# Kernel tuning notes

Hardware: AMD Instinct MI355X
Metric: run time of the kernel (lower is better)

Reference implementation:

```python
import jax, jax.numpy as jnp
import numpy as np
import math

N = 100000
E = 800000
H = 256
TDIM = 32
NTYPES = 22
NLAYERS = 2


def layer_norm(x, g, b, eps=1e-5):
    mu = jnp.mean(x, axis=-1, keepdims=True)
    var = jnp.var(x, axis=-1, keepdims=True)
    return (x - mu) * jax.lax.rsqrt(var + eps) * g + b


def setup_inputs() -> dict:
    key = jax.random.key(0)
    ks = jax.random.split(key, 16)
    s = 1.0 / math.sqrt(H)
    inp = {
        "clause_reprs": jax.random.normal(ks[0], (N, H), dtype=jnp.float32),
        "timestamps": jax.random.uniform(ks[1], (N,), dtype=jnp.float32) * 10000.0,
        "deriv_types": jax.random.randint(ks[2], (N,), 0, NTYPES),
        "derivation_edges": jax.random.randint(ks[3], (2, E), 0, N),
        # params
        "emb_table": jax.random.normal(ks[4], (NTYPES, H), dtype=jnp.float32),
        "temp_W": jax.random.normal(ks[5], (TDIM, H), dtype=jnp.float32) / math.sqrt(TDIM),
        "temp_b": jnp.zeros((H,), jnp.float32),
        "fus_W1": jax.random.normal(ks[6], (3 * H, H), dtype=jnp.float32) / math.sqrt(3 * H),
        "fus_b1": jnp.zeros((H,), jnp.float32),
        "fus_W2": jax.random.normal(ks[7], (H, H), dtype=jnp.float32) * s,
        "fus_b2": jnp.zeros((H,), jnp.float32),
        "in_g": jnp.ones((H,), jnp.float32),
        "in_b": jnp.zeros((H,), jnp.float32),
        "deriv_W": jax.random.normal(ks[8], (NLAYERS, 2 * H, H), dtype=jnp.float32) / math.sqrt(2 * H),
        "deriv_b": jnp.zeros((NLAYERS, H), jnp.float32),
        "dn_g": jnp.ones((NLAYERS, H), jnp.float32),
        "dn_b": jnp.zeros((NLAYERS, H), jnp.float32),
    }
    return inp


def reference(clause_reprs, timestamps, deriv_types, derivation_edges,
              emb_table, temp_W, temp_b, fus_W1, fus_b1, fus_W2, fus_b2,
              in_g, in_b, deriv_W, deriv_b, dn_g, dn_b):
    # --- temporal sinusoidal encoding -> projection ---
    half = TDIM // 2
    freqs = jnp.exp(-math.log(10000.0) * jnp.arange(half, dtype=jnp.float32) / half)
    angles = timestamps[:, None] * freqs[None, :]                      # (N, half)
    pe = jnp.concatenate([jnp.sin(angles), jnp.cos(angles)], axis=-1)  # (N, TDIM)
    temporal_enc = pe @ temp_W + temp_b                                # (N, H)
    # --- derivation type embedding ---
    deriv_enc = emb_table[deriv_types]                                 # (N, H)
    # --- input fusion + residual + LN ---
    cat = jnp.concatenate([clause_reprs, temporal_enc, deriv_enc], axis=-1)
    fused = jax.nn.relu(cat @ fus_W1 + fus_b1) @ fus_W2 + fus_b2
    x = layer_norm(fused + clause_reprs, in_g, in_b)
    # --- derivation message passing along DAG edges (parent -> child) ---
    src, dst = derivation_edges[0], derivation_edges[1]
    count = jnp.zeros((N, 1), jnp.float32).at[dst].add(1.0)
    count = jnp.maximum(count, 1.0)
    for l in range(NLAYERS):
        parent_msgs = x[src]                                           # (E, H) gather
        agg = jnp.zeros_like(x).at[dst].add(parent_msgs) / count       # (N, H) scatter-add
        combined = jnp.concatenate([x, agg], axis=-1)                  # (N, 2H)
        update = jax.nn.relu(combined @ deriv_W[l] + deriv_b[l])
        x = layer_norm(x + update, dn_g[l], dn_b[l])
    return x
```

## Files before the change

### kernel.cpp

```cpp
#include <hip/hip_runtime.h>
#include <hip/hip_bf16.h>
#include <math.h>

#define N_NODES 100000
#define N_EDGES 800000
#define H 256
#define NTYPES 22
#define SCAN_G 98
#define GRID5 ((N_NODES + 127) / 128)

typedef __attribute__((ext_vector_type(8))) short short8;
typedef __attribute__((ext_vector_type(4))) float f32x4;
typedef unsigned short u16;

__device__ __forceinline__ u16 f2bf(float f) {
    unsigned u = __float_as_uint(f);
    u += 0x7FFF + ((u >> 16) & 1);
    return (u16)(u >> 16);
}
__device__ __forceinline__ float bf2f(u16 u) {
    return __uint_as_float(((unsigned)u) << 16);
}
__device__ __forceinline__ int pi2(int k) {
    return (k & 192) | ((k & 3) << 4) | ((k >> 2) & 15);
}

__device__ __forceinline__ void gload16(const void* g, void* l) {
    __builtin_amdgcn_global_load_lds(
        (const __attribute__((address_space(1))) unsigned int*)g,
        (__attribute__((address_space(3))) unsigned int*)l, 16, 0, 0);
}

__global__ __launch_bounds__(256) void conv_bf16(
    const float* __restrict__ src, u16* __restrict__ dst)
{
    size_t i = (size_t)blockIdx.x * 256 + threadIdx.x;
    const float4 a = ((const float4*)src)[i * 2];
    const float4 b = ((const float4*)src)[i * 2 + 1];
    short8 v;
    v[0] = (short)f2bf(a.x); v[1] = (short)f2bf(a.y);
    v[2] = (short)f2bf(a.z); v[3] = (short)f2bf(a.w);
    v[4] = (short)f2bf(b.x); v[5] = (short)f2bf(b.y);
    v[6] = (short)f2bf(b.z); v[7] = (short)f2bf(b.w);
    ((short8*)dst)[i] = v;
}

__global__ __launch_bounds__(256) void prep_small(
    const float* __restrict__ temp_W, const float* __restrict__ temp_b,
    const float* __restrict__ emb, const float* __restrict__ fus_W1,
    const float* __restrict__ fus_b1,
    float* __restrict__ C1, float* __restrict__ C2, float* __restrict__ beff)
{
    int b = blockIdx.x;
    int j = threadIdx.x;
    if (b < 32) {
        float acc = 0.f;
        #pragma unroll 8
        for (int m = 0; m < H; ++m)
            acc += temp_W[b * H + m] * fus_W1[(size_t)(H + m) * H + j];
        C1[b * H + j] = acc;
    } else if (b < 32 + NTYPES) {
        int e = b - 32;
        float acc = 0.f;
        #pragma unroll 8
        for (int m = 0; m < H; ++m)
            acc += emb[e * H + m] * fus_W1[(size_t)(2 * H + m) * H + j];
        C2[e * H + j] = acc;
    } else {
        float acc = fus_b1[j];
        #pragma unroll 8
        for (int m = 0; m < H; ++m)
            acc += temp_b[m] * fus_W1[(size_t)(H + m) * H + j];
        beff[j] = acc;
    }
}

__global__ __launch_bounds__(256) void prep_frag(
    const float* __restrict__ fus_W1, const float* __restrict__ C1,
    const float* __restrict__ fus_W2, const float* __restrict__ deriv_W,
    u16* __restrict__ wblob)
{
    int s = blockIdx.x;
    #pragma unroll
    for (int it = 0; it < 4; ++it) {
        int c = it * 256 + threadIdx.x;
        int l = c & 63, nt = c >> 6;
        int ncol = (nt << 4) | (l & 15);
        int kin = (l >> 4) << 3;
        short8 v;
        #pragma unroll
        for (int i = 0; i < 8; ++i) {
            const float* srcp;
            if (s < 8) {
                srcp = fus_W1 + (size_t)(s * 32 + kin + i) * H;
            } else if (s == 8) {
                srcp = C1 + (size_t)(kin + i) * H;
            } else if (s < 17) {
                int k = (s - 9) * 32 + kin + i;
                srcp = fus_W2 + (size_t)pi2(k) * H;
            } else if (s < 33) {
                int k = (s - 17) * 32 + kin + i;
                srcp = deriv_W + (size_t)((k >> 8) * 256 + pi2(k & 255)) * H;
            } else {
                int k = (s - 33) * 32 + kin + i;
                srcp = deriv_W + (size_t)(512 + (k >> 8) * 256 + pi2(k & 255)) * H;
            }
            v[i] = (short)f2bf(srcp[ncol]);
        }
        *reinterpret_cast<short8*>(wblob + (size_t)s * 8192 + (size_t)c * 8) = v;
    }
}

__global__ void count_kernel(const int* __restrict__ dst, int* __restrict__ cnt)
{
    int e = blockIdx.x * blockDim.x + threadIdx.x;
    if (e < N_EDGES) atomicAdd(&cnt[dst[e]], 1);
}

__global__ __launch_bounds__(1024) void scan1_kernel(
    const int* __restrict__ cnt, int* __restrict__ off, int* __restrict__ bsum)
{
    __shared__ int s[1024];
    int i = blockIdx.x * 1024 + threadIdx.x;
    int v = (i < N_NODES) ? cnt[i] : 0;
    s[threadIdx.x] = v;
    __syncthreads();
    #pragma unroll
    for (int o = 1; o < 1024; o <<= 1) {
        int t = (threadIdx.x >= o) ? s[threadIdx.x - o] : 0;
        __syncthreads();
        s[threadIdx.x] += t;
        __syncthreads();
    }
    if (i < N_NODES) off[i] = s[threadIdx.x];
    if (threadIdx.x == 1023) bsum[blockIdx.x] = s[1023];
}

__global__ void scan2_kernel(const int* __restrict__ bsum, int* __restrict__ bbase)
{
    if (threadIdx.x == 0) {
        int acc = 0;
        for (int b = 0; b < SCAN_G; ++b) { bbase[b] = acc; acc += bsum[b]; }
    }
}

__global__ __launch_bounds__(1024) void scan3_kernel(
    int* __restrict__ off, const int* __restrict__ bbase,
    const int* __restrict__ cnt, int* __restrict__ cursor)
{
    int i = blockIdx.x * 1024 + threadIdx.x;
    if (i < N_NODES) {
        int incl = off[i] + bbase[blockIdx.x];
        off[i] = incl;
        cursor[i] = incl - cnt[i];
    }
}

__global__ void fill_kernel(const int* __restrict__ src, const int* __restrict__ dst,
                            int* __restrict__ cursor, int* __restrict__ csr)
{
    int e = blockIdx.x * blockDim.x + threadIdx.x;
    if (e < N_EDGES) {
        int pos = atomicAdd(&cursor[dst[e]], 1);
        csr[pos] = src[e];
    }
}

__global__ __launch_bounds__(256) void gather_kernel(
    const u16* __restrict__ xb, const int* __restrict__ csr,
    const int* __restrict__ off, const int* __restrict__ cnt,
    u16* __restrict__ agg)
{
    int node = blockIdx.x * 4 + (threadIdx.x >> 6);
    int l = threadIdx.x & 63;
    int half = l >> 5, lc = l & 31;
    int deg = cnt[node];
    int start = off[node] - deg;
    float a[8] = {0.f, 0.f, 0.f, 0.f, 0.f, 0.f, 0.f, 0.f};
    int j = half;
    for (; j + 2 < deg; j += 4) {
        int s0 = csr[start + j];
        int s1 = csr[start + j + 2];
        short8 v0 = *reinterpret_cast<const short8*>(xb + (size_t)s0 * H + lc * 8);
        short8 v1 = *reinterpret_cast<const short8*>(xb + (size_t)s1 * H + lc * 8);
        #pragma unroll
        for (int i = 0; i < 8; ++i)
            a[i] += bf2f((u16)v0[i]) + bf2f((u16)v1[i]);
    }
    if (j < deg) {
        int s0 = csr[start + j];
        short8 v0 = *reinterpret_cast<const short8*>(xb + (size_t)s0 * H + lc * 8);
        #pragma unroll
        for (int i = 0; i < 8; ++i)
            a[i] += bf2f((u16)v0[i]);
    }
    #pragma unroll
    for (int i = 0; i < 8; ++i)
        a[i] += __shfl_xor(a[i], 32);
    if (half == 0) {
        float sc = 1.0f / fmaxf((float)deg, 1.0f);
        short8 o;
        #pragma unroll
        for (int i = 0; i < 8; ++i) o[i] = (short)f2bf(a[i] * sc);
        *reinterpret_cast<short8*>(agg + (size_t)node * H + lc * 8) = o;
    }
}

__device__ __forceinline__ void stageA8(u16* Af, const u16* __restrict__ src,
                                        int i0, int kbase, int tid)
{
    int rt = tid >> 6, l = tid & 63;
    int row = min(i0 + rt * 16 + (l & 15), N_NODES - 1);
    gload16(src + (size_t)row * H + kbase + ((l >> 4) << 3), Af + (tid << 3));
}

__device__ __forceinline__ void stageB8(u16* Bf, const u16* __restrict__ wk, int tid)
{
    gload16(wk + ((size_t)tid << 3),         Bf + (tid << 3));
    gload16(wk + ((size_t)(tid + 512) << 3), Bf + ((tid + 512) << 3));
}

__device__ __forceinline__ void mfma_step8(const u16* Af, const u16* Bf,
                                           int wm, int wn, int l, f32x4 acc[4][4])
{
    short8 a[4], b[4];
    #pragma unroll
    for (int m = 0; m < 4; ++m)
        a[m] = *reinterpret_cast<const short8*>(Af + ((((wm << 2) | m) << 6 | l) << 3));
    #pragma unroll
    for (int n = 0; n < 4; ++n)
        b[n] = *reinterpret_cast<const short8*>(Bf + ((((wn << 2) | n) << 6 | l) << 3));
    #pragma unroll
    for (int n = 0; n < 4; ++n)
        #pragma unroll
        for (int m = 0; m < 4; ++m)
            acc[m][n] = __builtin_amdgcn_mfma_f32_16x16x32_bf16(a[m], b[n],
                                                                acc[m][n], 0, 0, 0);
}

__global__ __launch_bounds__(512, 4) void k1_mfma(
    const u16* __restrict__ cb, const float* __restrict__ ts,
    const int* __restrict__ types, const u16* __restrict__ wblob,
    const float* __restrict__ C2, const float* __restrict__ beff,
    u16* __restrict__ hb)
{
    __shared__ __align__(16) u16 Af[2][4096];
    __shared__ __align__(16) u16 Bf[2][8192];
    int tid = threadIdx.x, w = tid >> 6, l = tid & 63;
    int wm = w >> 2, wn = w & 3, g = l >> 4, c0 = l & 15;
    int i0 = blockIdx.x * 128;
    f32x4 acc[4][4] = {};

    stageA8(Af[0], cb, i0, 0, tid);
    stageB8(Bf[0], wblob, tid);
    __syncthreads();
    #pragma unroll
    for (int t = 0; t < 9; ++t) {
        int cur = t & 1;
        if (t < 8) {
            int t1 = t + 1;
            if (t1 < 8) {
                stageA8(Af[cur ^ 1], cb, i0, t1 * 32, tid);
            } else {
                int rt = tid >> 6;
                int row = min(i0 + rt * 16 + c0, N_NODES - 1);
                float tsv = ts[row];
                short8 v;
                #pragma unroll
                for (int i = 0; i < 8; ++i) {
                    int k = (g << 3) + i;
                    float fr = expf(-0.57564627324851f * (float)(k & 15));
                    float ang = tsv * fr;
                    float pv = (k < 16) ? sinf(ang) : cosf(ang);
                    v[i] = (short)f2bf(pv);
                }
                *reinterpret_cast<short8*>(Af[cur ^ 1] + (tid << 3)) = v;
            }
            stageB8(Bf[cur ^ 1], wblob + (size_t)t1 * 8192, tid);
        }
        mfma_step8(Af[cur], Bf[cur], wm, wn, l, acc);
        __syncthreads();
    }

    float bev[4];
    #pragma unroll
    for (int n = 0; n < 4; ++n) bev[n] = beff[(((wn << 2) | n) << 4) | c0];
    #pragma unroll
    for (int m = 0; m < 4; ++m) {
        #pragma unroll
        for (int r = 0; r < 4; ++r) {
            int rl = (((wm << 2) | m) << 4) + (g << 2) + r;
            int row = i0 + rl;
            bool ok = row < N_NODES;
            int tp = types[ok ? row : 0];
            const float* c2r = C2 + (size_t)tp * H;
            ushort4 o;
            float v0 = fmaxf(acc[m][0][r] + bev[0] + c2r[((wn << 2) << 4) | c0], 0.f);
            float v1 = fmaxf(acc[m][1][r] + bev[1] + c2r[(((wn << 2) | 1) << 4) | c0], 0.f);
            float v2 = fmaxf(acc[m][2][r] + bev[2] + c2r[(((wn << 2) | 2) << 4) | c0], 0.f);
            float v3 = fmaxf(acc[m][3][r] + bev[3] + c2r[(((wn << 2) | 3) << 4) | c0], 0.f);
            o.x = f2bf(v0); o.y = f2bf(v1); o.z = f2bf(v2); o.w = f2bf(v3);
            if (ok)
                *reinterpret_cast<ushort4*>(hb + (size_t)row * H + (wn << 6) + (c0 << 2)) = o;
        }
    }
}

__global__ __launch_bounds__(512, 4) void k2_mfma(
    const u16* __restrict__ hb, const u16* __restrict__ cb,
    const u16* __restrict__ wblob, const float* __restrict__ b2,
    const float* __restrict__ gW, const float* __restrict__ bW,
    u16* __restrict__ xb)
{
    __shared__ __align__(16) u16 Af[2][4096];
    __shared__ __align__(16) u16 Bf[2][8192];
    __shared__ float2 red[512];
    int tid = threadIdx.x, w = tid >> 6, l = tid & 63;
    int wm = w >> 2, wn = w & 3, g = l >> 4, c0 = l & 15;
    int i0 = blockIdx.x * 128;
    f32x4 acc[4][4] = {};

    stageA8(Af[0], hb, i0, 0, tid);
    stageB8(Bf[0], wblob, tid);
    __syncthreads();
    #pragma unroll
    for (int t = 0; t < 8; ++t) {
        int cur = t & 1;
        if (t < 7) {
            stageA8(Af[cur ^ 1], hb, i0, (t + 1) * 32, tid);
            stageB8(Bf[cur ^ 1], wblob + (size_t)(t + 1) * 8192, tid);
        }
        mfma_step8(Af[cur], Bf[cur], wm, wn, l, acc);
        __syncthreads();
    }

    float bv[4], gv[4], bbv[4];
    int lc[4];
    #pragma unroll
    for (int n = 0; n < 4; ++n) {
        lc[n] = (((wn << 2) | n) << 4) | c0;
        bv[n] = b2[lc[n]]; gv[n] = gW[lc[n]]; bbv[n] = bW[lc[n]];
    }
    #pragma unroll
    for (int m = 0; m < 4; ++m) {
        #pragma unroll
        for (int r = 0; r < 4; ++r) {
            int rl = (((wm << 2) | m) << 4) + (g << 2) + r;
            int rowc = min(i0 + rl, N_NODES - 1);
            const u16* cr = cb + (size_t)rowc * H;
            float s = 0.f, q = 0.f;
            #pragma unroll
            for (int n = 0; n < 4; ++n) {
                float pv = acc[m][n][r] + bv[n] + bf2f(cr[lc[n]]);
                acc[m][n][r] = pv;
                s += pv; q += pv * pv;
            }
            #pragma unroll
            for (int o = 1; o < 16; o <<= 1) {
                s += __shfl_xor(s, o);
                q += __shfl_xor(q, o);
            }
            if (c0 == 0) red[(rl << 2) | wn] = make_float2(s, q);
        }
    }
    __syncthreads();
    #pragma unroll
    for (int m = 0; m < 4; ++m) {
        #pragma unroll
        for (int r = 0; r < 4; ++r) {
            int rl = (((wm << 2) | m) << 4) + (g << 2) + r;
            int row = i0 + rl;
            float2 t0 = red[(rl << 2) | 0], t1 = red[(rl << 2) | 1];
            float2 t2 = red[(rl << 2) | 2], t3 = red[(rl << 2) | 3];
            float S = t0.x + t1.x + t2.x + t3.x;
            float Q = t0.y + t1.y + t2.y + t3.y;
            float mu = S * (1.0f / 256.0f);
            float rstd = rsqrtf(Q * (1.0f / 256.0f) - mu * mu + 1e-5f);
            if (row < N_NODES) {
                ushort4 o;
                o.x = f2bf((acc[m][0][r] - mu) * rstd * gv[0] + bbv[0]);
                o.y = f2bf((acc[m][1][r] - mu) * rstd * gv[1] + bbv[1]);
                o.z = f2bf((acc[m][2][r] - mu) * rstd * gv[2] + bbv[2]);
                o.w = f2bf((acc[m][3][r] - mu) * rstd * gv[3] + bbv[3]);
                *reinterpret_cast<ushort4*>(xb + (size_t)row * H + (wn << 6) + (c0 << 2)) = o;
            }
        }
    }
}

template<bool FINAL>
__global__ __launch_bounds__(512, 4) void k5_mfma(
    const u16* __restrict__ xb, const u16* __restrict__ aggb,
    const u16* __restrict__ wblob, const float* __restrict__ bl,
    const float* __restrict__ gl, const float* __restrict__ bnl,
    u16* __restrict__ xbout, float* __restrict__ xout)
{
    __shared__ __align__(16) u16 Af[2][4096];
    __shared__ __align__(16) u16 Bf[2][8192];
    __shared__ float2 red[512];
    int tid = threadIdx.x, w = tid >> 6, l = tid & 63;
    int wm = w >> 2, wn = w & 3, g = l >> 4, c0 = l & 15;
    int i0 = blockIdx.x * 128;
    f32x4 acc[4][4] = {};

    stageA8(Af[0], xb, i0, 0, tid);
    stageB8(Bf[0], wblob, tid);
    __syncthreads();
    #pragma unroll
    for (int t = 0; t < 16; ++t) {
        int cur = t & 1;
        if (t < 15) {
            int t1 = t + 1;
            stageA8(Af[cur ^ 1], (t1 < 8) ? xb : aggb, i0, (t1 & 7) * 32, tid);
            stageB8(Bf[cur ^ 1], wblob + (size_t)t1 * 8192, tid);
        }
        mfma_step8(Af[cur], Bf[cur], wm, wn, l, acc);
        __syncthreads();
    }

    float bv[4], gv[4], bbv[4];
    int lc[4];
    #pragma unroll
    for (int n = 0; n < 4; ++n) {
        lc[n] = (((wn << 2) | n) << 4) | c0;
        bv[n] = bl[lc[n]]; gv[n] = gl[lc[n]]; bbv[n] = bnl[lc[n]];
    }
    #pragma unroll
    for (int m = 0; m < 4; ++m) {
        #pragma unroll
        for (int r = 0; r < 4; ++r) {
            int rl = (((wm << 2) | m) << 4) + (g << 2) + r;
            int rowc = min(i0 + rl, N_NODES - 1);
            ushort4 xr = *reinterpret_cast<const ushort4*>(
                xb + (size_t)rowc * H + (wn << 6) + (c0 << 2));
            float p0 = bf2f(xr.x) + fmaxf(acc[m][0][r] + bv[0], 0.f);
            float p1 = bf2f(xr.y) + fmaxf(acc[m][1][r] + bv[1], 0.f);
            float p2 = bf2f(xr.z) + fmaxf(acc[m][2][r] + bv[2], 0.f);
            float p3 = bf2f(xr.w) + fmaxf(acc[m][3][r] + bv[3], 0.f);
            acc[m][0][r] = p0; acc[m][1][r] = p1;
            acc[m][2][r] = p2; acc[m][3][r] = p3;
            float s = p0 + p1 + p2 + p3;
            float q = p0 * p0 + p1 * p1 + p2 * p2 + p3 * p3;
            #pragma unroll
            for (int o = 1; o < 16; o <<= 1) {
                s += __shfl_xor(s, o);
                q += __shfl_xor(q, o);
            }
            if (c0 == 0) red[(rl << 2) | wn] = make_float2(s, q);
        }
    }
    __syncthreads();
    #pragma unroll
    for (int m = 0; m < 4; ++m) {
        #pragma unroll
        for (int r = 0; r < 4; ++r) {
            int rl = (((wm << 2) | m) << 4) + (g << 2) + r;
            int row = i0 + rl;
            float2 t0 = red[(rl << 2) | 0], t1 = red[(rl << 2) | 1];
            float2 t2 = red[(rl << 2) | 2], t3 = red[(rl << 2) | 3];
            float S = t0.x + t1.x + t2.x + t3.x;
            float Q = t0.y + t1.y + t2.y + t3.y;
            float mu = S * (1.0f / 256.0f);
            float rstd = rsqrtf(Q * (1.0f / 256.0f) - mu * mu + 1e-5f);
            if (row < N_NODES) {
                if (FINAL) {
                    #pragma unroll
                    for (int n = 0; n < 4; ++n)
                        xout[(size_t)row * H + lc[n]] =
                            (acc[m][n][r] - mu) * rstd * gv[n] + bbv[n];
                } else {
                    ushort4 o;
                    o.x = f2bf((acc[m][0][r] - mu) * rstd * gv[0] + bbv[0]);
                    o.y = f2bf((acc[m][1][r] - mu) * rstd * gv[1] + bbv[1]);
                    o.z = f2bf((acc[m][2][r] - mu) * rstd * gv[2] + bbv[2]);
                    o.w = f2bf((acc[m][3][r] - mu) * rstd * gv[3] + bbv[3]);
                    *reinterpret_cast<ushort4*>(
                        xbout + (size_t)row * H + (wn << 6) + (c0 << 2)) = o;
                }
            }
        }
    }
}

extern "C" void kernel_launch(void* const* d_in, const int* in_sizes, int n_in,
                              void* d_out, int out_size, void* d_ws, size_t ws_size,
                              hipStream_t stream)
{
    const float* clause  = (const float*)d_in[0];
    const float* ts      = (const float*)d_in[1];
    const int*   types   = (const int*)  d_in[2];
    const int*   edges   = (const int*)  d_in[3];
    const float* emb     = (const float*)d_in[4];
    const float* temp_W  = (const float*)d_in[5];
    const float* temp_b  = (const float*)d_in[6];
    const float* fus_W1  = (const float*)d_in[7];
    const float* fus_b1  = (const float*)d_in[8];
    const float* fus_W2  = (const float*)d_in[9];
    const float* fus_b2  = (const float*)d_in[10];
    const float* in_g    = (const float*)d_in[11];
    const float* in_b    = (const float*)d_in[12];
    const float* deriv_W = (const float*)d_in[13];
    const float* deriv_b = (const float*)d_in[14];
    const float* dn_g    = (const float*)d_in[15];
    const float* dn_b    = (const float*)d_in[16];

    char* p = (char*)d_ws;
    float* C1   = (float*)p;            p += 32 * H * 4;
    float* C2   = (float*)p;            p += NTYPES * H * 4;
    float* beff = (float*)p;            p += H * 4;
    int* cnt    = (int*)p;              p += N_NODES * 4;
    int* off    = (int*)p;              p += N_NODES * 4;
    int* cursor = (int*)p;              p += N_NODES * 4;
    int* bsum   = (int*)p;              p += 128 * 4;
    int* bbase  = (int*)p;              p += 128 * 4;
    int* csr    = (int*)p;              p += N_EDGES * 4;
    u16* wblob  = (u16*)p;              p += 49 * 8192 * 2;
    u16* B1     = (u16*)p;              p += (size_t)N_NODES * H * 2;
    u16* B2     = (u16*)p;              p += (size_t)N_NODES * H * 2;
    float* x    = (float*)d_out;

    const int* src = edges;
    const int* dst = edges + N_EDGES;

    conv_bf16<<<(N_NODES * H / 8 + 255) / 256, 256, 0, stream>>>(clause, B1);
    prep_small<<<32 + NTYPES + 1, 256, 0, stream>>>(temp_W, temp_b, emb, fus_W1,
                                                    fus_b1, C1, C2, beff);
    prep_frag<<<49, 256, 0, stream>>>(fus_W1, C1, fus_W2, deriv_W, wblob);

    hipMemsetAsync(cnt, 0, N_NODES * sizeof(int), stream);
    count_kernel<<<(N_EDGES + 255) / 256, 256, 0, stream>>>(dst, cnt);
    scan1_kernel<<<SCAN_G, 1024, 0, stream>>>(cnt, off, bsum);
    scan2_kernel<<<1, 64, 0, stream>>>(bsum, bbase);
    scan3_kernel<<<SCAN_G, 1024, 0, stream>>>(off, bbase, cnt, cursor);
    fill_kernel<<<(N_EDGES + 255) / 256, 256, 0, stream>>>(src, dst, cursor, csr);

    k1_mfma<<<GRID5, 512, 0, stream>>>(B1, ts, types, wblob, C2, beff, B2);
    k2_mfma<<<GRID5, 512, 0, stream>>>(B2, B1, wblob + (size_t)9 * 8192,
                                       fus_b2, in_g, in_b, B2);

    gather_kernel<<<N_NODES / 4, 256, 0, stream>>>(B2, csr, off, cnt, B1);
    k5_mfma<false><<<GRID5, 512, 0, stream>>>(
        B2, B1, wblob + (size_t)17 * 8192, deriv_b, dn_g, dn_b, B2, nullptr);
    gather_kernel<<<N_NODES / 4, 256, 0, stream>>>(B2, csr, off, cnt, B1);
    k5_mfma<true><<<GRID5, 512, 0, stream>>>(
        B2, B1, wblob + (size_t)33 * 8192, deriv_b + H, dn_g + H, dn_b + H,
        nullptr, x);
}
```

Measured before the change: 572.9 us.

## Stage full A tile in swizzled LDS once, stream weights directly from global

The three MFMA GEMM kernels no longer double-buffer 32-wide K slices of A and B through LDS with a barrier every step. Each now loads the block's entire 128-row A tile into XOR-swizzled LDS once (plus a precomputed sinusoidal tile in k1), then reads B fragments straight from global/L2 into registers with no barriers inside the K loop. k5 also reuses the staged x rows from LDS for the residual instead of reloading them from global. The cost is much larger LDS use (128KB in k5, with launch bounds lowered to 2), lower occupancy, and no overlap between the A load and the MFMA work.

New measurement: 580.8 us. No clear change (+1.4%).

```diff
diff --git a/kernel.cpp b/kernel.cpp
--- a/kernel.cpp
+++ b/kernel.cpp
@@ -206,30 +206,9 @@
     }
 }
 
-__device__ __forceinline__ void stageA8(u16* Af, const u16* __restrict__ src,
-                                        int i0, int kbase, int tid)
-{
-    int rt = tid >> 6, l = tid & 63;
-    int row = min(i0 + rt * 16 + (l & 15), N_NODES - 1);
-    gload16(src + (size_t)row * H + kbase + ((l >> 4) << 3), Af + (tid << 3));
-}
-
-__device__ __forceinline__ void stageB8(u16* Bf, const u16* __restrict__ wk, int tid)
-{
-    gload16(wk + ((size_t)tid << 3),         Bf + (tid << 3));
-    gload16(wk + ((size_t)(tid + 512) << 3), Bf + ((tid + 512) << 3));
-}
-
-__device__ __forceinline__ void mfma_step8(const u16* Af, const u16* Bf,
-                                           int wm, int wn, int l, f32x4 acc[4][4])
-{
-    short8 a[4], b[4];
-    #pragma unroll
-    for (int m = 0; m < 4; ++m)
-        a[m] = *reinterpret_cast<const short8*>(Af + ((((wm << 2) | m) << 6 | l) << 3));
-    #pragma unroll
-    for (int n = 0; n < 4; ++n)
-        b[n] = *reinterpret_cast<const short8*>(Bf + ((((wn << 2) | n) << 6 | l) << 3));
+__device__ __forceinline__ void mfma_regs(const short8 a[4], const short8 b[4],
+                                          f32x4 acc[4][4])
+{
     #pragma unroll
     for (int n = 0; n < 4; ++n)
         #pragma unroll
@@ -244,42 +223,56 @@
     const float* __restrict__ C2, const float* __restrict__ beff,
     u16* __restrict__ hb)
 {
-    __shared__ __align__(16) u16 Af[2][4096];
-    __shared__ __align__(16) u16 Bf[2][8192];
+    __shared__ __align__(16) u16 Asm[32768];
+    __shared__ __align__(16) u16 pes[4096];
     int tid = threadIdx.x, w = tid >> 6, l = tid & 63;
     int wm = w >> 2, wn = w & 3, g = l >> 4, c0 = l & 15;
     int i0 = blockIdx.x * 128;
+
+    #pragma unroll
+    for (int j = 0; j < 8; ++j) {
+        int rt = j * 16 + (tid >> 5);
+        int grow = min(i0 + rt, N_NODES - 1);
+        int gl = (l & 31) ^ (rt & 7);
+        gload16(cb + (size_t)grow * H + gl * 8,
+                Asm + (size_t)rt * 256 + (l & 31) * 8);
+    }
+    {
+        int prow = tid >> 2, kq = tid & 3;
+        float tsv = ts[min(i0 + prow, N_NODES - 1)];
+        short8 v;
+        #pragma unroll
+        for (int i = 0; i < 8; ++i) {
+            int k = kq * 8 + i;
+            float fr = expf(-0.57564627324851f * (float)(k & 15));
+            float ang = tsv * fr;
+            v[i] = (short)f2bf((k < 16) ? sinf(ang) : cosf(ang));
+        }
+        *reinterpret_cast<short8*>(pes + prow * 32 + ((kq ^ (prow & 3)) << 3)) = v;
+    }
+    __syncthreads();
+
     f32x4 acc[4][4] = {};
-
-    stageA8(Af[0], cb, i0, 0, tid);
-    stageB8(Bf[0], wblob, tid);
-    __syncthreads();
     #pragma unroll
     for (int t = 0; t < 9; ++t) {
-        int cur = t & 1;
-        if (t < 8) {
-            int t1 = t + 1;
-            if (t1 < 8) {
-                stageA8(Af[cur ^ 1], cb, i0, t1 * 32, tid);
+        short8 a[4], b[4];
+        #pragma unroll
+        for (int m = 0; m < 4; ++m) {
+            int row = (((wm << 2) | m) << 4) + c0;
+            if (t < 8) {
+                int c = t * 4 + g;
+                a[m] = *reinterpret_cast<const short8*>(
+                    Asm + row * 256 + ((c ^ (c0 & 7)) << 3));
             } else {
-                int rt = tid >> 6;
-                int row = min(i0 + rt * 16 + c0, N_NODES - 1);
-                float tsv = ts[row];
-                short8 v;
-                #pragma unroll
-                for (int i = 0; i < 8; ++i) {
-                    int k = (g << 3) + i;
-                    float fr = expf(-0.57564627324851f * (float)(k & 15));
-                    float ang = tsv * fr;
-                    float pv = (k < 16) ? sinf(ang) : cosf(ang);
-                    v[i] = (short)f2bf(pv);
-                }
-                *reinterpret_cast<short8*>(Af[cur ^ 1] + (tid << 3)) = v;
-            }
-            stageB8(Bf[cur ^ 1], wblob + (size_t)t1 * 8192, tid);
-        }
-        mfma_step8(Af[cur], Bf[cur], wm, wn, l, acc);
-        __syncthreads();
+                a[m] = *reinterpret_cast<const short8*>(
+                    pes + row * 32 + ((g ^ (c0 & 3)) << 3));
+            }
+        }
+        #pragma unroll
+        for (int n = 0; n < 4; ++n)
+            b[n] = *reinterpret_cast<const short8*>(
+                wblob + (size_t)t * 8192 + (size_t)(((((wn << 2) | n) << 6) | l) << 3));
+        mfma_regs(a, b, acc);
     }
 
     float bev[4];
@@ -312,26 +305,38 @@
     const float* __restrict__ gW, const float* __restrict__ bW,
     u16* __restrict__ xb)
 {
-    __shared__ __align__(16) u16 Af[2][4096];
-    __shared__ __align__(16) u16 Bf[2][8192];
+    __shared__ __align__(16) u16 Asm[32768];
     __shared__ float2 red[512];
     int tid = threadIdx.x, w = tid >> 6, l = tid & 63;
     int wm = w >> 2, wn = w & 3, g = l >> 4, c0 = l & 15;
     int i0 = blockIdx.x * 128;
+
+    #pragma unroll
+    for (int j = 0; j < 8; ++j) {
+        int rt = j * 16 + (tid >> 5);
+        int grow = min(i0 + rt, N_NODES - 1);
+        int gl = (l & 31) ^ (rt & 7);
+        gload16(hb + (size_t)grow * H + gl * 8,
+                Asm + (size_t)rt * 256 + (l & 31) * 8);
+    }
+    __syncthreads();
+
     f32x4 acc[4][4] = {};
-
-    stageA8(Af[0], hb, i0, 0, tid);
-    stageB8(Bf[0], wblob, tid);
-    __syncthreads();
     #pragma unroll
     for (int t = 0; t < 8; ++t) {
-        int cur = t & 1;
-        if (t < 7) {
-            stageA8(Af[cur ^ 1], hb, i0, (t + 1) * 32, tid);
-            stageB8(Bf[cur ^ 1], wblob + (size_t)(t + 1) * 8192, tid);
-        }
-        mfma_step8(Af[cur], Bf[cur], wm, wn, l, acc);
-        __syncthreads();
+        short8 a[4], b[4];
+        #pragma unroll
+        for (int m = 0; m < 4; ++m) {
+            int row = (((wm << 2) | m) << 4) + c0;
+            int c = t * 4 + g;
+            a[m] = *reinterpret_cast<const short8*>(
+                Asm + row * 256 + ((c ^ (c0 & 7)) << 3));
+        }
+        #pragma unroll
+        for (int n = 0; n < 4; ++n)
+            b[n] = *reinterpret_cast<const short8*>(
+                wblob + (size_t)t * 8192 + (size_t)(((((wn << 2) | n) << 6) | l) << 3));
+        mfma_regs(a, b, acc);
     }
 
     float bv[4], gv[4], bbv[4];
@@ -389,33 +394,46 @@
 }
 
 template<bool FINAL>
-__global__ __launch_bounds__(512, 4) void k5_mfma(
+__global__ __launch_bounds__(512, 2) void k5_mfma(
     const u16* __restrict__ xb, const u16* __restrict__ aggb,
     const u16* __restrict__ wblob, const float* __restrict__ bl,
-    const float* __restrict__ gl, const float* __restrict__ bnl,
+    const float* __restrict__ gl_, const float* __restrict__ bnl,
     u16* __restrict__ xbout, float* __restrict__ xout)
 {
-    __shared__ __align__(16) u16 Af[2][4096];
-    __shared__ __align__(16) u16 Bf[2][8192];
+    __shared__ __align__(16) u16 Asm[65536];
     __shared__ float2 red[512];
     int tid = threadIdx.x, w = tid >> 6, l = tid & 63;
     int wm = w >> 2, wn = w & 3, g = l >> 4, c0 = l & 15;
     int i0 = blockIdx.x * 128;
+
+    #pragma unroll
+    for (int j = 0; j < 16; ++j) {
+        int rt = j * 8 + w;
+        int grow = min(i0 + rt, N_NODES - 1);
+        int gl = l ^ w;
+        const u16* src = (gl < 32)
+            ? xb + (size_t)grow * H + gl * 8
+            : aggb + (size_t)grow * H + (gl - 32) * 8;
+        gload16(src, Asm + (size_t)rt * 512 + l * 8);
+    }
+    __syncthreads();
+
     f32x4 acc[4][4] = {};
-
-    stageA8(Af[0], xb, i0, 0, tid);
-    stageB8(Bf[0], wblob, tid);
-    __syncthreads();
     #pragma unroll
     for (int t = 0; t < 16; ++t) {
-        int cur = t & 1;
-        if (t < 15) {
-            int t1 = t + 1;
-            stageA8(Af[cur ^ 1], (t1 < 8) ? xb : aggb, i0, (t1 & 7) * 32, tid);
-            stageB8(Bf[cur ^ 1], wblob + (size_t)t1 * 8192, tid);
-        }
-        mfma_step8(Af[cur], Bf[cur], wm, wn, l, acc);
-        __syncthreads();
+        short8 a[4], b[4];
+        #pragma unroll
+        for (int m = 0; m < 4; ++m) {
+            int row = (((wm << 2) | m) << 4) + c0;
+            int c = t * 4 + g;
+            a[m] = *reinterpret_cast<const short8*>(
+                Asm + row * 512 + ((c ^ (c0 & 7)) << 3));
+        }
+        #pragma unroll
+        for (int n = 0; n < 4; ++n)
+            b[n] = *reinterpret_cast<const short8*>(
+                wblob + (size_t)t * 8192 + (size_t)(((((wn << 2) | n) << 6) | l) << 3));
+        mfma_regs(a, b, acc);
     }
 
     float bv[4], gv[4], bbv[4];
@@ -423,16 +441,16 @@
     #pragma unroll
     for (int n = 0; n < 4; ++n) {
         lc[n] = (((wn << 2) | n) << 4) | c0;
-        bv[n] = bl[lc[n]]; gv[n] = gl[lc[n]]; bbv[n] = bnl[lc[n]];
-    }
+        bv[n] = bl[lc[n]]; gv[n] = gl_[lc[n]]; bbv[n] = bnl[lc[n]];
+    }
+    int g0 = (wn << 3) + (c0 >> 1);
     #pragma unroll
     for (int m = 0; m < 4; ++m) {
         #pragma unroll
         for (int r = 0; r < 4; ++r) {
             int rl = (((wm << 2) | m) << 4) + (g << 2) + r;
-            int rowc = min(i0 + rl, N_NODES - 1);
             ushort4 xr = *reinterpret_cast<const ushort4*>(
-                xb + (size_t)rowc * H + (wn << 6) + (c0 << 2));
+                Asm + rl * 512 + ((g0 ^ (rl & 7)) << 3) + ((c0 & 1) << 2));
             float p0 = bf2f(xr.x) + fmaxf(acc[m][0][r] + bv[0], 0.f);
             float p1 = bf2f(xr.y) + fmaxf(acc[m][1][r] + bv[1], 0.f);
             float p2 = bf2f(xr.z) + fmaxf(acc[m][2][r] + bv[2], 0.f);
```

## Use partial vmcnt waits and split barriers in MFMA GEMM pipelines

Applied to the files above, without the earlier changes.

Replaces the full __syncthreads in the double-buffered GEMM loops of k1, k2 and k5 with explicit s_waitcnt vmcnt(N) plus s_barrier. Each stage now waits only for the previous stage's async LDS loads while the next stage's loads stay in flight. It also raises wave priority around the MFMA block and hoists k1's sinusoidal encoding computation ahead of the loop. The hand-counted vmcnt values depend on how many loads the compiler emits per stage, so a miscount could cause races.

Result: faster. 532.4 us (-7.1%).

```diff
diff --git a/kernel.cpp b/kernel.cpp
--- a/kernel.cpp
+++ b/kernel.cpp
@@ -30,6 +30,17 @@
         (const __attribute__((address_space(1))) unsigned int*)g,
         (__attribute__((address_space(3))) unsigned int*)l, 16, 0, 0);
 }
+
+#define BAR_WAIT3()  do { __builtin_amdgcn_sched_barrier(0); \
+    asm volatile("s_waitcnt vmcnt(3)\ns_barrier" ::: "memory"); } while (0)
+#define BAR_WAIT2()  do { __builtin_amdgcn_sched_barrier(0); \
+    asm volatile("s_waitcnt vmcnt(2)\ns_barrier" ::: "memory"); } while (0)
+#define BAR_WAIT0()  do { __builtin_amdgcn_sched_barrier(0); \
+    asm volatile("s_waitcnt vmcnt(0)\ns_barrier" ::: "memory"); } while (0)
+#define BAR_WAIT0L() do { __builtin_amdgcn_sched_barrier(0); \
+    asm volatile("s_waitcnt vmcnt(0) lgkmcnt(0)\ns_barrier" ::: "memory"); } while (0)
+#define BAR_REL()    do { __builtin_amdgcn_sched_barrier(0); \
+    asm volatile("s_barrier" ::: "memory"); } while (0)
 
 __global__ __launch_bounds__(256) void conv_bf16(
     const float* __restrict__ src, u16* __restrict__ dst)
@@ -230,12 +241,14 @@
     #pragma unroll
     for (int n = 0; n < 4; ++n)
         b[n] = *reinterpret_cast<const short8*>(Bf + ((((wn << 2) | n) << 6 | l) << 3));
+    __builtin_amdgcn_s_setprio(1);
     #pragma unroll
     for (int n = 0; n < 4; ++n)
         #pragma unroll
         for (int m = 0; m < 4; ++m)
             acc[m][n] = __builtin_amdgcn_mfma_f32_16x16x32_bf16(a[m], b[n],
                                                                 acc[m][n], 0, 0, 0);
+    __builtin_amdgcn_s_setprio(0);
 }
 
 __global__ __launch_bounds__(512, 4) void k1_mfma(
@@ -248,38 +261,38 @@
     __shared__ __align__(16) u16 Bf[2][8192];
     int tid = threadIdx.x, w = tid >> 6, l = tid & 63;
     int wm = w >> 2, wn = w & 3, g = l >> 4, c0 = l & 15;
+    int kg = g << 3;
     int i0 = blockIdx.x * 128;
     f32x4 acc[4][4] = {};
 
+    short8 pv;
+    {
+        float tsv = ts[min(i0 + ((w << 4) | c0), N_NODES - 1)];
+        #pragma unroll
+        for (int i = 0; i < 8; ++i) {
+            int k = kg + i;
+            float fr = expf(-0.57564627324851f * (float)(k & 15));
+            float ang = tsv * fr;
+            pv[i] = (short)f2bf((k < 16) ? sinf(ang) : cosf(ang));
+        }
+    }
+
     stageA8(Af[0], cb, i0, 0, tid);
     stageB8(Bf[0], wblob, tid);
-    __syncthreads();
     #pragma unroll
     for (int t = 0; t < 9; ++t) {
         int cur = t & 1;
         if (t < 8) {
-            int t1 = t + 1;
-            if (t1 < 8) {
-                stageA8(Af[cur ^ 1], cb, i0, t1 * 32, tid);
-            } else {
-                int rt = tid >> 6;
-                int row = min(i0 + rt * 16 + c0, N_NODES - 1);
-                float tsv = ts[row];
-                short8 v;
-                #pragma unroll
-                for (int i = 0; i < 8; ++i) {
-                    int k = (g << 3) + i;
-                    float fr = expf(-0.57564627324851f * (float)(k & 15));
-                    float ang = tsv * fr;
-                    float pv = (k < 16) ? sinf(ang) : cosf(ang);
-                    v[i] = (short)f2bf(pv);
-                }
-                *reinterpret_cast<short8*>(Af[cur ^ 1] + (tid << 3)) = v;
-            }
-            stageB8(Bf[cur ^ 1], wblob + (size_t)t1 * 8192, tid);
-        }
+            if (t < 7) stageA8(Af[cur ^ 1], cb, i0, (t + 1) * 32, tid);
+            stageB8(Bf[cur ^ 1], wblob + (size_t)(t + 1) * 8192, tid);
+        }
+        if (t == 8)
+            *reinterpret_cast<short8*>(Af[0] + (tid << 3)) = pv;
+        if (t < 7)       BAR_WAIT3();
+        else if (t == 7) BAR_WAIT2();
+        else             BAR_WAIT0L();
         mfma_step8(Af[cur], Bf[cur], wm, wn, l, acc);
-        __syncthreads();
+        BAR_REL();
     }
 
     float bev[4];
@@ -322,7 +335,6 @@
 
     stageA8(Af[0], hb, i0, 0, tid);
     stageB8(Bf[0], wblob, tid);
-    __syncthreads();
     #pragma unroll
     for (int t = 0; t < 8; ++t) {
         int cur = t & 1;
@@ -330,8 +342,9 @@
             stageA8(Af[cur ^ 1], hb, i0, (t + 1) * 32, tid);
             stageB8(Bf[cur ^ 1], wblob + (size_t)(t + 1) * 8192, tid);
         }
+        if (t < 7) BAR_WAIT3(); else BAR_WAIT0();
         mfma_step8(Af[cur], Bf[cur], wm, wn, l, acc);
-        __syncthreads();
+        BAR_REL();
     }
 
     float bv[4], gv[4], bbv[4];
@@ -392,7 +405,7 @@
 __global__ __launch_bounds__(512, 4) void k5_mfma(
     const u16* __restrict__ xb, const u16* __restrict__ aggb,
     const u16* __restrict__ wblob, const float* __restrict__ bl,
-    const float* __restrict__ gl, const float* __restrict__ bnl,
+    const float* __restrict__ gl_, const float* __restrict__ bnl,
     u16* __restrict__ xbout, float* __restrict__ xout)
 {
     __shared__ __align__(16) u16 Af[2][4096];
@@ -405,7 +418,6 @@
 
     stageA8(Af[0], xb, i0, 0, tid);
     stageB8(Bf[0], wblob, tid);
-    __syncthreads();
     #pragma unroll
     for (int t = 0; t < 16; ++t) {
         int cur = t & 1;
@@ -414,8 +426,9 @@
             stageA8(Af[cur ^ 1], (t1 < 8) ? xb : aggb, i0, (t1 & 7) * 32, tid);
             stageB8(Bf[cur ^ 1], wblob + (size_t)t1 * 8192, tid);
         }
+        if (t < 15) BAR_WAIT3(); else BAR_WAIT0();
         mfma_step8(Af[cur], Bf[cur], wm, wn, l, acc);
-        __syncthreads();
+        BAR_REL();
     }
 
     float bv[4], gv[4], bbv[4];
@@ -423,7 +436,7 @@
     #pragma unroll
     for (int n = 0; n < 4; ++n) {
         lc[n] = (((wn << 2) | n) << 4) | c0;
-        bv[n] = bl[lc[n]]; gv[n] = gl[lc[n]]; bbv[n] = bnl[lc[n]];
+        bv[n] = bl[lc[n]]; gv[n] = gl_[lc[n]]; bbv[n] = bnl[lc[n]];
     }
     #pragma unroll
     for (int m = 0; m < 4; ++m) {
```
